# Performance work log

Measured on AMD Instinct MI355X. Metric: run time of the kernel, lower is better.

## Reference

```python
import jax, jax.numpy as jnp
import numpy as np

FP16_MAX = 65504.0  # clamp_fp16 bound
GROUP = 64          # SVDQuant int4 group size along in_features


def _int4_quant_dequant(w):
    """Symmetric per-(out_channel, group) int4 fake-quant of a weight [out, in].
    Emulates the W4 weight numerics of SVDQW4A4Linear at the dequantized level."""
    o, i = w.shape
    wg = w.reshape(o, i // GROUP, GROUP)
    scale = np.max(np.abs(wg), axis=-1, keepdims=True) / 7.0
    scale = np.where(scale == 0.0, 1.0, scale)
    q = np.clip(np.round(wg / scale), -8, 7)
    return (q * scale).reshape(o, i).astype(np.float32)


def setup_inputs() -> dict:
    dim, hidden = 3072, 8192
    B, S = 2, 4096
    rng = np.random.default_rng(0)
    # fused [w1; w3] weight: [2*hidden, dim]; down proj w2: [dim, hidden]
    w13 = _int4_quant_dequant((rng.standard_normal((2 * hidden, dim)) * 0.02).astype(np.float32))
    w2 = _int4_quant_dequant((rng.standard_normal((dim, hidden)) * 0.02).astype(np.float32))
    key = jax.random.key(0)
    x = jax.random.normal(key, (B, S, dim), dtype=jnp.float32)
    return {"x": x, "w13": jnp.asarray(w13), "w2": jnp.asarray(w2)}


def reference(x, w13, w2):
    # fused gate/up projection: [B,S,dim] @ [2H,dim]^T -> [B,S,2H]
    h = jnp.einsum("bsd,hd->bsh", x, w13)
    # NOTE: original code does `x3, x1 = x.chunk(2, dim=-1)` -> first half is x3
    x3, x1 = jnp.split(h, 2, axis=-1)
    g = jnp.clip(jax.nn.silu(x1) * x3, -FP16_MAX, FP16_MAX)  # clamp_fp16
    # down projection: [B,S,H] @ [dim,H]^T -> [B,S,dim]
    return jnp.einsum("bsh,dh->bsd", g, w2)
```

## Files before the change

### kernel.cpp

```cpp
#include <hip/hip_runtime.h>
#include <hip/hip_bf16.h>


typedef __attribute__((ext_vector_type(8))) __bf16 bf16x8;
typedef __attribute__((ext_vector_type(16))) float f32x16;

#define GLD_LDS16(gptr, lptr)                                                        \
  __builtin_amdgcn_global_load_lds(                                                  \
      (const __attribute__((address_space(1))) void*)(gptr),                         \
      (__attribute__((address_space(3))) void*)(lptr), 16, 0, 0)

#define VMCNT(n) asm volatile("s_waitcnt vmcnt(" #n ")" ::: "memory")
#define FENCE()  asm volatile("" ::: "memory")

__device__ __forceinline__ __bf16 bfr(float f) {
  unsigned int u = __builtin_bit_cast(unsigned int, f);
  unsigned short r = (unsigned short)((u + 0x7FFFu + ((u >> 16) & 1u)) >> 16);
  return __builtin_bit_cast(__bf16, r);
}

__global__ __launch_bounds__(256)
void k_cvt(const float* __restrict__ src, unsigned short* __restrict__ dst, long n) {
  long i = ((long)blockIdx.x * 256 + threadIdx.x) * 8;
  const long stride = (long)gridDim.x * 256 * 8;
  for (; i < n; i += stride) {
    float4 f0 = *(const float4*)(src + i);
    float4 f1 = *(const float4*)(src + i + 4);
    bf16x8 o;
    o[0] = bfr(f0.x); o[1] = bfr(f0.y); o[2] = bfr(f0.z); o[3] = bfr(f0.w);
    o[4] = bfr(f1.x); o[5] = bfr(f1.y); o[6] = bfr(f1.z); o[7] = bfr(f1.w);
    *(bf16x8*)(dst + i) = o;
  }
}

__global__ __launch_bounds__(512, 2)
void k_gateup10(const unsigned short* __restrict__ X,
                const unsigned short* __restrict__ W13,
                __hip_bfloat16* __restrict__ G)
{
  constexpr int K = 3072, LDG = 8192, NT = K / 32;
  __shared__ unsigned short lds[4 * 16384];

  const int t = threadIdx.x;
  const int l = t & 63, wid = t >> 6;
  const int wm = wid >> 2, wn = wid & 3;
  const int l31 = l & 31, lh = l >> 5;
  const int sw2 = (l31 >> 1) & 3;

  const int bid = blockIdx.x;
  const int swz = (bid & 7) * 256 + (bid >> 3);
  const int mb = swz >> 6, nb = swz & 63;

  const int srow = t >> 2;
  const int scol = ((t & 3) ^ ((srow >> 1) & 3)) * 8;
  const unsigned short* xa = X   + (size_t)(mb * 256 + srow) * K + scol;
  const unsigned short* b3 = W13 + (size_t)(nb * 128 + srow) * K + scol;
  const unsigned short* b1 = W13 + (size_t)(8192 + nb * 128 + srow) * K + scol;
  const int lo = t * 8;

  f32x16 acc3[4], acc1[4];
#pragma unroll
  for (int mf = 0; mf < 4; ++mf)
#pragma unroll
    for (int r = 0; r < 16; ++r) { acc3[mf][r] = 0.f; acc1[mf][r] = 0.f; }

#pragma unroll
  for (int tt = 0; tt < 3; ++tt) {
    unsigned short* S = lds + tt * 16384;
    const int kt = tt * 32;
    GLD_LDS16(xa + kt, S + lo);
    GLD_LDS16(xa + (size_t)128 * K + kt, S + 4096 + lo);
    GLD_LDS16(b3 + kt, S + 8192 + lo);
    GLD_LDS16(b1 + kt, S + 12288 + lo);
  }

  for (int tk = 0; tk < NT; ++tk) {
    unsigned short* A = lds + (tk & 3) * 16384;
    unsigned short* S = lds + ((tk + 3) & 3) * 16384;
    const int ksrc = (tk + 3 < NT ? tk + 3 : 0) * 32;

    VMCNT(8);
    __builtin_amdgcn_s_barrier();
    FENCE();

    bf16x8 ra[4][2], r3[2], r1[2];
#pragma unroll
    for (int mf = 0; mf < 4; ++mf)
#pragma unroll
      for (int ks = 0; ks < 2; ++ks) {
        const int row = wm * 128 + mf * 32 + l31;
        ra[mf][ks] = *(const bf16x8*)(A + row * 32 + (((ks * 2 + lh) ^ sw2) * 8));
      }
#pragma unroll
    for (int ks = 0; ks < 2; ++ks) {
      const int row = wn * 32 + l31;
      const int sl = ((ks * 2 + lh) ^ sw2) * 8;
      r3[ks] = *(const bf16x8*)(A + 8192 + row * 32 + sl);
      r1[ks] = *(const bf16x8*)(A + 12288 + row * 32 + sl);
    }

    GLD_LDS16(xa + ksrc, S + lo);
    GLD_LDS16(xa + (size_t)128 * K + ksrc, S + 4096 + lo);
    GLD_LDS16(b3 + ksrc, S + 8192 + lo);
    GLD_LDS16(b1 + ksrc, S + 12288 + lo);

    __builtin_amdgcn_s_setprio(1);
#pragma unroll
    for (int ks = 0; ks < 2; ++ks)
#pragma unroll
      for (int mf = 0; mf < 4; ++mf) {
        acc3[mf] = __builtin_amdgcn_mfma_f32_32x32x16_bf16(ra[mf][ks], r3[ks], acc3[mf], 0, 0, 0);
        acc1[mf] = __builtin_amdgcn_mfma_f32_32x32x16_bf16(ra[mf][ks], r1[ks], acc1[mf], 0, 0, 0);
      }
    __builtin_amdgcn_s_setprio(0);
  }

  const int gr0 = mb * 256 + wm * 128;
  const int gc  = nb * 128 + wn * 32 + l31;
#pragma unroll
  for (int mf = 0; mf < 4; ++mf)
#pragma unroll
    for (int r = 0; r < 16; ++r) {
      const int row = gr0 + mf * 32 + (r & 3) + 8 * (r >> 2) + 4 * lh;
      float h3 = acc3[mf][r], h1 = acc1[mf][r];
      float s  = h1 / (1.f + __expf(-h1));
      float g  = fminf(fmaxf(s * h3, -65504.f), 65504.f);
      G[(size_t)row * LDG + gc] = __float2bfloat16(g);
    }
}

__global__ __launch_bounds__(512, 2)
void k_down10(const unsigned short* __restrict__ Gm,
              const unsigned short* __restrict__ W2,
              float* __restrict__ Out)
{
  constexpr int K = 8192, LDO = 3072, NT = K / 64;
  __shared__ unsigned short lds[3 * 24576];

  const int t = threadIdx.x;
  const int l = t & 63, wid = t >> 6;
  const int wm = wid >> 1, wn = wid & 1;
  const int l31 = l & 31, lh = l >> 5;
  const int sw = l31 & 7;

  const int bid = blockIdx.x;
  const int swz = (bid & 7) * 96 + (bid >> 3);
  const int mb = swz / 24, nb = swz % 24;

  const int srow = t >> 3;
  const int scol = ((t & 7) ^ (srow & 7)) * 8;
  const unsigned short* ga = Gm + (size_t)(mb * 256 + srow) * K + scol;
  const unsigned short* wb = W2 + (size_t)(nb * 128 + srow) * K + scol;
  const int lo = t * 8;

  f32x16 acc[2][2];
#pragma unroll
  for (int mf = 0; mf < 2; ++mf)
#pragma unroll
    for (int nf = 0; nf < 2; ++nf)
#pragma unroll
      for (int r = 0; r < 16; ++r) acc[mf][nf][r] = 0.f;

#pragma unroll
  for (int tt = 0; tt < 2; ++tt) {
    unsigned short* S = lds + tt * 24576;
    const int kt = tt * 64;
#pragma unroll
    for (int q = 0; q < 4; ++q)
      GLD_LDS16(ga + (size_t)(q * 64) * K + kt, S + q * 4096 + lo);
#pragma unroll
    for (int h = 0; h < 2; ++h)
      GLD_LDS16(wb + (size_t)(h * 64) * K + kt, S + 16384 + h * 4096 + lo);
  }

  for (int tk = 0; tk < NT; ++tk) {
    unsigned short* A = lds + (tk % 3) * 24576;
    unsigned short* S = lds + ((tk + 2) % 3) * 24576;
    const int ksrc = (tk + 2 < NT ? tk + 2 : 0) * 64;

    VMCNT(6);
    __builtin_amdgcn_s_barrier();
    FENCE();

    bf16x8 ra[2][4], rb[2][4];
#pragma unroll
    for (int mf = 0; mf < 2; ++mf)
#pragma unroll
      for (int ks = 0; ks < 4; ++ks) {
        const int row = wm * 64 + mf * 32 + l31;
        ra[mf][ks] = *(const bf16x8*)(A + row * 64 + (((ks * 2 + lh) ^ sw) * 8));
      }
#pragma unroll
    for (int nf = 0; nf < 2; ++nf)
#pragma unroll
      for (int ks = 0; ks < 4; ++ks) {
        const int row = wn * 64 + nf * 32 + l31;
        rb[nf][ks] = *(const bf16x8*)(A + 16384 + row * 64 + (((ks * 2 + lh) ^ sw) * 8));
      }

#pragma unroll
    for (int q = 0; q < 4; ++q)
      GLD_LDS16(ga + (size_t)(q * 64) * K + ksrc, S + q * 4096 + lo);
#pragma unroll
    for (int h = 0; h < 2; ++h)
      GLD_LDS16(wb + (size_t)(h * 64) * K + ksrc, S + 16384 + h * 4096 + lo);

    __builtin_amdgcn_s_setprio(1);
#pragma unroll
    for (int ks = 0; ks < 4; ++ks)
#pragma unroll
      for (int mf = 0; mf < 2; ++mf)
#pragma unroll
        for (int nf = 0; nf < 2; ++nf)
          acc[mf][nf] = __builtin_amdgcn_mfma_f32_32x32x16_bf16(ra[mf][ks], rb[nf][ks], acc[mf][nf], 0, 0, 0);
    __builtin_amdgcn_s_setprio(0);
  }

  const int r0 = mb * 256 + wm * 64;
  const int c0 = nb * 128 + wn * 64;
#pragma unroll
  for (int mf = 0; mf < 2; ++mf)
#pragma unroll
    for (int nf = 0; nf < 2; ++nf)
#pragma unroll
      for (int r = 0; r < 16; ++r) {
        const int row = r0 + mf * 32 + (r & 3) + 8 * (r >> 2) + 4 * lh;
        Out[(size_t)row * LDO + c0 + nf * 32 + l31] = acc[mf][nf][r];
      }
}

extern "C" void kernel_launch(void* const* d_in, const int* in_sizes, int n_in,
                              void* d_out, int out_size, void* d_ws, size_t ws_size,
                              hipStream_t stream) {
  const float* x   = (const float*)d_in[0];
  const float* w13 = (const float*)d_in[1];
  const float* w2  = (const float*)d_in[2];
  float* out = (float*)d_out;

  const long NX = 25165824L, NW13 = 50331648L, NW2 = 25165824L;
  const size_t XB = 50331648, W13B = 100663296, W2B = 50331648;

  unsigned short* xb   = (unsigned short*)d_ws;
  unsigned short* w13b = (unsigned short*)((char*)d_ws + XB);
  unsigned short* w2b  = (unsigned short*)((char*)d_ws + XB + W13B);
  __hip_bfloat16* g    = (__hip_bfloat16*)((char*)d_ws + XB + W13B + W2B);

  k_cvt<<<2048, 256, 0, stream>>>(x,   xb,   NX);
  k_cvt<<<2048, 256, 0, stream>>>(w13, w13b, NW13);
  k_cvt<<<2048, 256, 0, stream>>>(w2,  w2b,  NW2);
  k_gateup10<<<2048, 512, 0, stream>>>(xb, w13b, g);
  k_down10<<<768, 512, 0, stream>>>((const unsigned short*)g, w2b, out);
}
```

Before: 1.348 ms.

## Switch GEMMs to 16x16x32 MFMA with interleaved ping-pong load/compute phases

Both GEMM kernels move from 32x32x16 to 16x16x32 bf16 MFMA tiles, and the K-tile grows to 64 with an 8-way XOR swizzle. The gate/up kernel now double-buffers LDS and splits each K step into four barrier-separated sub-phases. Each sub-phase issues one quarter of the next global-to-LDS loads while running one quadrant of MFMAs, so memory traffic interleaves with compute. This raises the number of barriers and changes the register layout, so results depend on how well the fine-grained schedule hides latency.

```diff
diff --git a/kernel.cpp b/kernel.cpp
--- a/kernel.cpp
+++ b/kernel.cpp
@@ -3,7 +3,7 @@
 
 
 typedef __attribute__((ext_vector_type(8))) __bf16 bf16x8;
-typedef __attribute__((ext_vector_type(16))) float f32x16;
+typedef __attribute__((ext_vector_type(4))) float f32x4;
 
 #define GLD_LDS16(gptr, lptr)                                                        \
   __builtin_amdgcn_global_load_lds(                                                  \
@@ -11,7 +11,9 @@
       (__attribute__((address_space(3))) void*)(lptr), 16, 0, 0)
 
 #define VMCNT(n) asm volatile("s_waitcnt vmcnt(" #n ")" ::: "memory")
-#define FENCE()  asm volatile("" ::: "memory")
+#define BAR()    __builtin_amdgcn_s_barrier()
+
+#define MFMA16(a, b, c) __builtin_amdgcn_mfma_f32_16x16x32_bf16((a), (b), (c), 0, 0, 0)
 
 __device__ __forceinline__ __bf16 bfr(float f) {
   unsigned int u = __builtin_bit_cast(unsigned int, f);
@@ -34,114 +36,175 @@
 }
 
 __global__ __launch_bounds__(512, 2)
-void k_gateup10(const unsigned short* __restrict__ X,
+void k_gateup11(const unsigned short* __restrict__ X,
                 const unsigned short* __restrict__ W13,
                 __hip_bfloat16* __restrict__ G)
 {
-  constexpr int K = 3072, LDG = 8192, NT = K / 32;
-  __shared__ unsigned short lds[4 * 16384];
-
-  const int t = threadIdx.x;
-  const int l = t & 63, wid = t >> 6;
+  constexpr int K = 3072, LDG = 8192, NT = K / 64;
+  __shared__ unsigned short lds[65536];
+
+  const int t = threadIdx.x, l = t & 63, wid = t >> 6;
   const int wm = wid >> 2, wn = wid & 3;
-  const int l31 = l & 31, lh = l >> 5;
-  const int sw2 = (l31 >> 1) & 3;
+  const int l15 = l & 15, lhi = l >> 4, sw = l15 & 7;
 
   const int bid = blockIdx.x;
   const int swz = (bid & 7) * 256 + (bid >> 3);
   const int mb = swz >> 6, nb = swz & 63;
 
-  const int srow = t >> 2;
-  const int scol = ((t & 3) ^ ((srow >> 1) & 3)) * 8;
+  const int srow = t >> 3;
+  const int scol = ((t & 7) ^ (srow & 7)) * 8;
   const unsigned short* xa = X   + (size_t)(mb * 256 + srow) * K + scol;
   const unsigned short* b3 = W13 + (size_t)(nb * 128 + srow) * K + scol;
   const unsigned short* b1 = W13 + (size_t)(8192 + nb * 128 + srow) * K + scol;
   const int lo = t * 8;
 
-  f32x16 acc3[4], acc1[4];
-#pragma unroll
-  for (int mf = 0; mf < 4; ++mf)
-#pragma unroll
-    for (int r = 0; r < 16; ++r) { acc3[mf][r] = 0.f; acc1[mf][r] = 0.f; }
-
-#pragma unroll
-  for (int tt = 0; tt < 3; ++tt) {
-    unsigned short* S = lds + tt * 16384;
-    const int kt = tt * 32;
-    GLD_LDS16(xa + kt, S + lo);
-    GLD_LDS16(xa + (size_t)128 * K + kt, S + 4096 + lo);
-    GLD_LDS16(b3 + kt, S + 8192 + lo);
-    GLD_LDS16(b1 + kt, S + 12288 + lo);
+#define ST_A02(d, kt) do {                                                     \
+    GLD_LDS16(xa + (kt),                 lds + (d) * 16384 + lo);              \
+    GLD_LDS16(xa + (size_t)128 * K + (kt), lds + (d) * 16384 + 8192 + lo);     \
+  } while (0)
+#define ST_A13(d, kt) do {                                                     \
+    GLD_LDS16(xa + (size_t)64 * K + (kt),  lds + (d) * 16384 + 4096 + lo);     \
+    GLD_LDS16(xa + (size_t)192 * K + (kt), lds + (d) * 16384 + 12288 + lo);    \
+  } while (0)
+#define ST_B3(d, kt) do {                                                      \
+    GLD_LDS16(b3 + (kt),                lds + 32768 + (d) * 8192 + lo);        \
+    GLD_LDS16(b3 + (size_t)64 * K + (kt), lds + 32768 + (d) * 8192 + 4096 + lo); \
+  } while (0)
+#define ST_B1(d, kt) do {                                                      \
+    GLD_LDS16(b1 + (kt),                lds + 49152 + (d) * 8192 + lo);        \
+    GLD_LDS16(b1 + (size_t)64 * K + (kt), lds + 49152 + (d) * 8192 + 4096 + lo); \
+  } while (0)
+
+  f32x4 acc3[8][2], acc1[8][2];
+#pragma unroll
+  for (int m = 0; m < 8; ++m)
+#pragma unroll
+    for (int n = 0; n < 2; ++n) {
+      acc3[m][n] = (f32x4){0.f, 0.f, 0.f, 0.f};
+      acc1[m][n] = (f32x4){0.f, 0.f, 0.f, 0.f};
+    }
+
+  ST_B3(0, 0); ST_A02(0, 0); ST_B1(0, 0); ST_A13(0, 0);
+  ST_B3(1, 64); ST_A02(1, 64); ST_B1(1, 64);
+  VMCNT(6);
+  BAR();
+
+  for (int c = 0; c < NT; ++c) {
+    const int d = c & 1, dn = d ^ 1;
+    const int k1 = (c + 1 < NT ? c + 1 : 0) * 64;
+    const int k2 = (c + 2 < NT ? c + 2 : 0) * 64;
+    const int Ab = d * 16384, B3b = 32768 + d * 8192, B1b = 49152 + d * 8192;
+
+    bf16x8 ra[4][2], rb[4][2], r3[2][2], r1[2][2];
+
+#pragma unroll
+    for (int mf = 0; mf < 4; ++mf)
+#pragma unroll
+      for (int kk = 0; kk < 2; ++kk)
+        ra[mf][kk] = *(const bf16x8*)(lds + Ab + (wm * 128 + mf * 16 + l15) * 64 + ((kk * 4 + lhi) ^ sw) * 8);
+#pragma unroll
+    for (int nf = 0; nf < 2; ++nf)
+#pragma unroll
+      for (int kk = 0; kk < 2; ++kk)
+        r3[nf][kk] = *(const bf16x8*)(lds + B3b + (wn * 32 + nf * 16 + l15) * 64 + ((kk * 4 + lhi) ^ sw) * 8);
+    ST_A13(dn, k1);
+    BAR();
+    __builtin_amdgcn_s_setprio(1);
+#pragma unroll
+    for (int mf = 0; mf < 4; ++mf)
+#pragma unroll
+      for (int nf = 0; nf < 2; ++nf)
+#pragma unroll
+        for (int kk = 0; kk < 2; ++kk)
+          acc3[mf][nf] = MFMA16(ra[mf][kk], r3[nf][kk], acc3[mf][nf]);
+    __builtin_amdgcn_s_setprio(0);
+    BAR();
+
+#pragma unroll
+    for (int nf = 0; nf < 2; ++nf)
+#pragma unroll
+      for (int kk = 0; kk < 2; ++kk)
+        r1[nf][kk] = *(const bf16x8*)(lds + B1b + (wn * 32 + nf * 16 + l15) * 64 + ((kk * 4 + lhi) ^ sw) * 8);
+    ST_B3(d, k2);
+    BAR();
+    __builtin_amdgcn_s_setprio(1);
+#pragma unroll
+    for (int mf = 0; mf < 4; ++mf)
+#pragma unroll
+      for (int nf = 0; nf < 2; ++nf)
+#pragma unroll
+        for (int kk = 0; kk < 2; ++kk)
+          acc1[mf][nf] = MFMA16(ra[mf][kk], r1[nf][kk], acc1[mf][nf]);
+    __builtin_amdgcn_s_setprio(0);
+    BAR();
+
+#pragma unroll
+    for (int mf = 0; mf < 4; ++mf)
+#pragma unroll
+      for (int kk = 0; kk < 2; ++kk)
+        rb[mf][kk] = *(const bf16x8*)(lds + Ab + (wm * 128 + 64 + mf * 16 + l15) * 64 + ((kk * 4 + lhi) ^ sw) * 8);
+    ST_A02(d, k2);
+    BAR();
+    __builtin_amdgcn_s_setprio(1);
+#pragma unroll
+    for (int mf = 0; mf < 4; ++mf)
+#pragma unroll
+      for (int nf = 0; nf < 2; ++nf)
+#pragma unroll
+        for (int kk = 0; kk < 2; ++kk)
+          acc3[4 + mf][nf] = MFMA16(rb[mf][kk], r3[nf][kk], acc3[4 + mf][nf]);
+    __builtin_amdgcn_s_setprio(0);
+    BAR();
+
+    ST_B1(d, k2);
+    VMCNT(6);
+    BAR();
+    __builtin_amdgcn_s_setprio(1);
+#pragma unroll
+    for (int mf = 0; mf < 4; ++mf)
+#pragma unroll
+      for (int nf = 0; nf < 2; ++nf)
+#pragma unroll
+        for (int kk = 0; kk < 2; ++kk)
+          acc1[4 + mf][nf] = MFMA16(rb[mf][kk], r1[nf][kk], acc1[4 + mf][nf]);
+    __builtin_amdgcn_s_setprio(0);
+    BAR();
   }
 
-  for (int tk = 0; tk < NT; ++tk) {
-    unsigned short* A = lds + (tk & 3) * 16384;
-    unsigned short* S = lds + ((tk + 3) & 3) * 16384;
-    const int ksrc = (tk + 3 < NT ? tk + 3 : 0) * 32;
-
-    VMCNT(8);
-    __builtin_amdgcn_s_barrier();
-    FENCE();
-
-    bf16x8 ra[4][2], r3[2], r1[2];
-#pragma unroll
-    for (int mf = 0; mf < 4; ++mf)
-#pragma unroll
-      for (int ks = 0; ks < 2; ++ks) {
-        const int row = wm * 128 + mf * 32 + l31;
-        ra[mf][ks] = *(const bf16x8*)(A + row * 32 + (((ks * 2 + lh) ^ sw2) * 8));
+  const int gr0 = mb * 256 + wm * 128;
+  const int gc0 = nb * 128 + wn * 32;
+#pragma unroll
+  for (int mf = 0; mf < 8; ++mf) {
+    const int ro = (mf >> 2) * 64 + (mf & 3) * 16;
+#pragma unroll
+    for (int nf = 0; nf < 2; ++nf)
+#pragma unroll
+      for (int r = 0; r < 4; ++r) {
+        float h3 = acc3[mf][nf][r];
+        float h1 = acc1[mf][nf][r];
+        float s  = h1 / (1.f + __expf(-h1));
+        float g  = fminf(fmaxf(s * h3, -65504.f), 65504.f);
+        G[(size_t)(gr0 + ro + lhi * 4 + r) * LDG + (gc0 + nf * 16 + l15)] =
+            __float2bfloat16(g);
       }
-#pragma unroll
-    for (int ks = 0; ks < 2; ++ks) {
-      const int row = wn * 32 + l31;
-      const int sl = ((ks * 2 + lh) ^ sw2) * 8;
-      r3[ks] = *(const bf16x8*)(A + 8192 + row * 32 + sl);
-      r1[ks] = *(const bf16x8*)(A + 12288 + row * 32 + sl);
-    }
-
-    GLD_LDS16(xa + ksrc, S + lo);
-    GLD_LDS16(xa + (size_t)128 * K + ksrc, S + 4096 + lo);
-    GLD_LDS16(b3 + ksrc, S + 8192 + lo);
-    GLD_LDS16(b1 + ksrc, S + 12288 + lo);
-
-    __builtin_amdgcn_s_setprio(1);
-#pragma unroll
-    for (int ks = 0; ks < 2; ++ks)
-#pragma unroll
-      for (int mf = 0; mf < 4; ++mf) {
-        acc3[mf] = __builtin_amdgcn_mfma_f32_32x32x16_bf16(ra[mf][ks], r3[ks], acc3[mf], 0, 0, 0);
-        acc1[mf] = __builtin_amdgcn_mfma_f32_32x32x16_bf16(ra[mf][ks], r1[ks], acc1[mf], 0, 0, 0);
-      }
-    __builtin_amdgcn_s_setprio(0);
   }
-
-  const int gr0 = mb * 256 + wm * 128;
-  const int gc  = nb * 128 + wn * 32 + l31;
-#pragma unroll
-  for (int mf = 0; mf < 4; ++mf)
-#pragma unroll
-    for (int r = 0; r < 16; ++r) {
-      const int row = gr0 + mf * 32 + (r & 3) + 8 * (r >> 2) + 4 * lh;
-      float h3 = acc3[mf][r], h1 = acc1[mf][r];
-      float s  = h1 / (1.f + __expf(-h1));
-      float g  = fminf(fmaxf(s * h3, -65504.f), 65504.f);
-      G[(size_t)row * LDG + gc] = __float2bfloat16(g);
-    }
+#undef ST_A02
+#undef ST_A13
+#undef ST_B3
+#undef ST_B1
 }
 
 __global__ __launch_bounds__(512, 2)
-void k_down10(const unsigned short* __restrict__ Gm,
+void k_down11(const unsigned short* __restrict__ Gm,
               const unsigned short* __restrict__ W2,
               float* __restrict__ Out)
 {
   constexpr int K = 8192, LDO = 3072, NT = K / 64;
-  __shared__ unsigned short lds[3 * 24576];
-
-  const int t = threadIdx.x;
-  const int l = t & 63, wid = t >> 6;
+  __shared__ unsigned short lds[73728];
+
+  const int t = threadIdx.x, l = t & 63, wid = t >> 6;
   const int wm = wid >> 1, wn = wid & 1;
-  const int l31 = l & 31, lh = l >> 5;
-  const int sw = l31 & 7;
+  const int l15 = l & 15, lhi = l >> 4, sw = l15 & 7;
 
   const int bid = blockIdx.x;
   const int swz = (bid & 7) * 96 + (bid >> 3);
@@ -153,80 +216,73 @@
   const unsigned short* wb = W2 + (size_t)(nb * 128 + srow) * K + scol;
   const int lo = t * 8;
 
-  f32x16 acc[2][2];
-#pragma unroll
-  for (int mf = 0; mf < 2; ++mf)
-#pragma unroll
-    for (int nf = 0; nf < 2; ++nf)
-#pragma unroll
-      for (int r = 0; r < 16; ++r) acc[mf][nf][r] = 0.f;
-
-#pragma unroll
-  for (int tt = 0; tt < 2; ++tt) {
-    unsigned short* S = lds + tt * 24576;
-    const int kt = tt * 64;
-#pragma unroll
-    for (int q = 0; q < 4; ++q)
-      GLD_LDS16(ga + (size_t)(q * 64) * K + kt, S + q * 4096 + lo);
-#pragma unroll
-    for (int h = 0; h < 2; ++h)
-      GLD_LDS16(wb + (size_t)(h * 64) * K + kt, S + 16384 + h * 4096 + lo);
-  }
-
-  for (int tk = 0; tk < NT; ++tk) {
-    unsigned short* A = lds + (tk % 3) * 24576;
-    unsigned short* S = lds + ((tk + 2) % 3) * 24576;
-    const int ksrc = (tk + 2 < NT ? tk + 2 : 0) * 64;
+#define DST_A(e, kt) do {                                                       \
+    GLD_LDS16(ga + (kt),                 lds + (e) * 16384 + lo);               \
+    GLD_LDS16(ga + (size_t)64 * K + (kt),  lds + (e) * 16384 + 4096 + lo);      \
+    GLD_LDS16(ga + (size_t)128 * K + (kt), lds + (e) * 16384 + 8192 + lo);      \
+    GLD_LDS16(ga + (size_t)192 * K + (kt), lds + (e) * 16384 + 12288 + lo);     \
+  } while (0)
+#define DST_B(e, kt) do {                                                       \
+    GLD_LDS16(wb + (kt),                lds + 49152 + (e) * 8192 + lo);         \
+    GLD_LDS16(wb + (size_t)64 * K + (kt), lds + 49152 + (e) * 8192 + 4096 + lo); \
+  } while (0)
+
+  f32x4 acc[4][4];
+#pragma unroll
+  for (int mf = 0; mf < 4; ++mf)
+#pragma unroll
+    for (int nf = 0; nf < 4; ++nf)
+      acc[mf][nf] = (f32x4){0.f, 0.f, 0.f, 0.f};
+
+  DST_B(0, 0);  DST_A(0, 0);
+  DST_B(1, 64); DST_A(1, 64);
+
+  for (int c = 0; c < NT; ++c) {
+    const int e = c % 3;
+    const int eS = (c + 2) % 3;
+    const int k2 = (c + 2 < NT ? c + 2 : 0) * 64;
 
     VMCNT(6);
-    __builtin_amdgcn_s_barrier();
-    FENCE();
-
-    bf16x8 ra[2][4], rb[2][4];
-#pragma unroll
-    for (int mf = 0; mf < 2; ++mf)
-#pragma unroll
-      for (int ks = 0; ks < 4; ++ks) {
-        const int row = wm * 64 + mf * 32 + l31;
-        ra[mf][ks] = *(const bf16x8*)(A + row * 64 + (((ks * 2 + lh) ^ sw) * 8));
-      }
-#pragma unroll
-    for (int nf = 0; nf < 2; ++nf)
-#pragma unroll
-      for (int ks = 0; ks < 4; ++ks) {
-        const int row = wn * 64 + nf * 32 + l31;
-        rb[nf][ks] = *(const bf16x8*)(A + 16384 + row * 64 + (((ks * 2 + lh) ^ sw) * 8));
-      }
-
-#pragma unroll
-    for (int q = 0; q < 4; ++q)
-      GLD_LDS16(ga + (size_t)(q * 64) * K + ksrc, S + q * 4096 + lo);
-#pragma unroll
-    for (int h = 0; h < 2; ++h)
-      GLD_LDS16(wb + (size_t)(h * 64) * K + ksrc, S + 16384 + h * 4096 + lo);
-
-    __builtin_amdgcn_s_setprio(1);
-#pragma unroll
-    for (int ks = 0; ks < 4; ++ks)
-#pragma unroll
-      for (int mf = 0; mf < 2; ++mf)
-#pragma unroll
-        for (int nf = 0; nf < 2; ++nf)
-          acc[mf][nf] = __builtin_amdgcn_mfma_f32_32x32x16_bf16(ra[mf][ks], rb[nf][ks], acc[mf][nf], 0, 0, 0);
+    BAR();
+
+    bf16x8 ra[4][2], rb[4][2];
+#pragma unroll
+    for (int mf = 0; mf < 4; ++mf)
+#pragma unroll
+      for (int kk = 0; kk < 2; ++kk)
+        ra[mf][kk] = *(const bf16x8*)(lds + e * 16384 + (wm * 64 + mf * 16 + l15) * 64 + ((kk * 4 + lhi) ^ sw) * 8);
+#pragma unroll
+    for (int nf = 0; nf < 4; ++nf)
+#pragma unroll
+      for (int kk = 0; kk < 2; ++kk)
+        rb[nf][kk] = *(const bf16x8*)(lds + 49152 + e * 8192 + (wn * 64 + nf * 16 + l15) * 64 + ((kk * 4 + lhi) ^ sw) * 8);
+
+    DST_B(eS, k2);
+    DST_A(eS, k2);
+
+    __builtin_amdgcn_s_setprio(1);
+#pragma unroll
+    for (int mf = 0; mf < 4; ++mf)
+#pragma unroll
+      for (int nf = 0; nf < 4; ++nf)
+#pragma unroll
+        for (int kk = 0; kk < 2; ++kk)
+          acc[mf][nf] = MFMA16(ra[mf][kk], rb[nf][kk], acc[mf][nf]);
     __builtin_amdgcn_s_setprio(0);
   }
 
   const int r0 = mb * 256 + wm * 64;
   const int c0 = nb * 128 + wn * 64;
 #pragma unroll
-  for (int mf = 0; mf < 2; ++mf)
-#pragma unroll
-    for (int nf = 0; nf < 2; ++nf)
-#pragma unroll
-      for (int r = 0; r < 16; ++r) {
-        const int row = r0 + mf * 32 + (r & 3) + 8 * (r >> 2) + 4 * lh;
-        Out[(size_t)row * LDO + c0 + nf * 32 + l31] = acc[mf][nf][r];
-      }
+  for (int mf = 0; mf < 4; ++mf)
+#pragma unroll
+    for (int nf = 0; nf < 4; ++nf)
+#pragma unroll
+      for (int r = 0; r < 4; ++r)
+        Out[(size_t)(r0 + mf * 16 + lhi * 4 + r) * LDO + (c0 + nf * 16 + l15)] =
+            acc[mf][nf][r];
+#undef DST_A
+#undef DST_B
 }
 
 extern "C" void kernel_launch(void* const* d_in, const int* in_sizes, int n_in,
@@ -248,6 +304,6 @@
   k_cvt<<<2048, 256, 0, stream>>>(x,   xb,   NX);
   k_cvt<<<2048, 256, 0, stream>>>(w13, w13b, NW13);
   k_cvt<<<2048, 256, 0, stream>>>(w2,  w2b,  NW2);
-  k_gateup10<<<2048, 512, 0, stream>>>(xb, w13b, g);
-  k_down10<<<768, 512, 0, stream>>>((const unsigned short*)g, w2b, out);
-}
+  k_gateup11<<<2048, 512, 0, stream>>>(xb, w13b, g);
+  k_down11<<<768, 512, 0, stream>>>((const unsigned short*)g, w2b, out);
+}
```

New measurement: 1.195 ms. -11.3%, faster.
